# Kernel tuning notes

Hardware: AMD Instinct MI355X
Metric: run time of the kernel (lower is better)

## Reference

```python
import jax, jax.numpy as jnp
import numpy as np

QMIN, QMAX = -128.0, 127.0  # int8 range


def setup_inputs() -> dict:
    key = jax.random.key(0)
    k1, k2, k3 = jax.random.split(key, 3)
    B, S, IN, OUT = 4, 2048, 4096, 4096
    x = jax.random.normal(k1, (B, S, IN), dtype=jnp.float32)
    quantized_weight = jax.random.randint(k2, (OUT, IN), -128, 128, dtype=jnp.int32)
    weight_scale = jnp.float32(0.01)
    activation_scale = jnp.float32(0.05)
    bias = jax.random.normal(k3, (OUT,), dtype=jnp.float32)
    return {
        "x": x,
        "quantized_weight": quantized_weight,
        "weight_scale": weight_scale,
        "activation_scale": activation_scale,
        "bias": bias,
    }


def reference(x, quantized_weight, weight_scale, activation_scale, bias):
    # Fake-quantize activations to int8 grid (round, clamp), then dequantize.
    x_q = jnp.clip(jnp.round(x / activation_scale), QMIN, QMAX)
    x_f = x_q * activation_scale  # [B,S,IN] fp32
    # Dequantize int8 weights.
    w_f = quantized_weight.astype(jnp.float32) * weight_scale  # [OUT,IN]
    # F.linear: x @ W^T + b
    out = jnp.einsum("bsi,oi->bso", x_f, w_f) + bias
    return out
```

## Files before the change

kernel.cpp:

```cpp
#include <hip/hip_runtime.h>


#define MD 8192
#define ND 4096
#define KD 4096
#define KT (KD / 64)

typedef int   int4v   __attribute__((ext_vector_type(4)));
typedef float float4v __attribute__((ext_vector_type(4)));


__device__ __forceinline__ int quant1(float v, float s) {
  float q = rintf(v / s);
  q = fmaxf(-128.0f, fminf(127.0f, q));
  return ((int)q) & 0xff;
}

__global__ __launch_bounds__(256) void quant_x_kernel(
    const float* __restrict__ x, const float* __restrict__ as_p,
    signed char* __restrict__ aq) {
  const float s = as_p[0];
  int tid  = blockIdx.x * 256 + threadIdx.x;
  int sub  = tid >> 6;
  int lane = tid & 63;
  int mt = sub / KT;
  int kt = sub - mt * KT;
  int m = mt * 16 + (lane & 15);
  int k = kt * 64 + (lane >> 4) * 16;
  const float* src = x + (size_t)m * KD + k;
  int4v o;
#pragma unroll
  for (int i = 0; i < 4; ++i) {
    float4v v = *(const float4v*)(src + i * 4);
    o[i] = quant1(v.x, s) | (quant1(v.y, s) << 8) |
           (quant1(v.z, s) << 16) | (quant1(v.w, s) << 24);
  }
  *(int4v*)(aq + (size_t)sub * 1024 + lane * 16) = o;
}

__global__ __launch_bounds__(256) void pack_w_kernel(
    const int* __restrict__ w, signed char* __restrict__ wq) {
  int tid  = blockIdx.x * 256 + threadIdx.x;
  int sub  = tid >> 6;
  int lane = tid & 63;
  int nt = sub / KT;
  int kt = sub - nt * KT;
  int n = nt * 16 + (lane & 15);
  int k = kt * 64 + (lane >> 4) * 16;
  const int* src = w + (size_t)n * KD + k;
  int4v o;
#pragma unroll
  for (int i = 0; i < 4; ++i) {
    int4v v = *(const int4v*)(src + i * 4);
    o[i] = (v.x & 0xff) | ((v.y & 0xff) << 8) |
           ((v.z & 0xff) << 16) | ((v.w & 0xff) << 24);
  }
  *(int4v*)(wq + (size_t)sub * 1024 + lane * 16) = o;
}

__global__ __launch_bounds__(256) void gemm_i8_kernel(
    const signed char* __restrict__ aq, const signed char* __restrict__ wq,
    const float* __restrict__ ws_p, const float* __restrict__ as_p,
    const float* __restrict__ bias, float* __restrict__ out) {
  __shared__ signed char lds_a[8192];
  __shared__ signed char lds_b[8192];

  int nwg = gridDim.x;
  int cpx = nwg >> 3;
  int bid = blockIdx.x;
  int wg  = (bid & 7) * cpx + (bid >> 3);
  const int NT = ND / 128;
  int tm = wg / NT;
  int tn = wg - tm * NT;

  int tid  = threadIdx.x;
  int lane = tid & 63;
  int wv   = tid >> 6;
  int wr   = wv >> 1;
  int wc   = wv & 1;

  const size_t a_base = (size_t)(tm * 8) * KT * 1024;
  const size_t b_base = (size_t)(tn * 8) * KT * 1024;

  int4v acc[4][4];
#pragma unroll
  for (int i = 0; i < 4; ++i)
#pragma unroll
    for (int j = 0; j < 4; ++j) acc[i][j] = (int4v){0, 0, 0, 0};

  for (int kt = 0; kt < KT; ++kt) {
#pragma unroll
    for (int j = 0; j < 2; ++j) {
      int ia = wv + j * 4;
      const signed char* ga = aq + a_base + ((size_t)ia * KT + kt) * 1024 + lane * 16;
      __builtin_amdgcn_global_load_lds(
          (const __attribute__((address_space(1))) void*)ga,
          (__attribute__((address_space(3))) void*)(lds_a + ia * 1024), 16, 0, 0);
      const signed char* gb = wq + b_base + ((size_t)ia * KT + kt) * 1024 + lane * 16;
      __builtin_amdgcn_global_load_lds(
          (const __attribute__((address_space(1))) void*)gb,
          (__attribute__((address_space(3))) void*)(lds_b + ia * 1024), 16, 0, 0);
    }
    __syncthreads();

    int4v afrag[4], bfrag[4];
#pragma unroll
    for (int rb = 0; rb < 4; ++rb)
      afrag[rb] = *(const int4v*)(lds_a + (wr * 4 + rb) * 1024 + lane * 16);
#pragma unroll
    for (int cb = 0; cb < 4; ++cb)
      bfrag[cb] = *(const int4v*)(lds_b + (wc * 4 + cb) * 1024 + lane * 16);

#pragma unroll
    for (int rb = 0; rb < 4; ++rb)
#pragma unroll
      for (int cb = 0; cb < 4; ++cb)
        acc[rb][cb] = __builtin_amdgcn_mfma_i32_16x16x64_i8(
            afrag[rb], bfrag[cb], acc[rb][cb], 0, 0, 0);

    __syncthreads();
  }

  float scale = ws_p[0] * as_p[0];
  int col0 = tn * 128 + wc * 64 + (lane & 15);
  int row0 = tm * 128 + wr * 64 + ((lane >> 4) << 2);
  float bv[4];
#pragma unroll
  for (int cb = 0; cb < 4; ++cb) bv[cb] = bias[col0 + cb * 16];
#pragma unroll
  for (int rb = 0; rb < 4; ++rb) {
#pragma unroll
    for (int cb = 0; cb < 4; ++cb) {
      int col = col0 + cb * 16;
#pragma unroll
      for (int j = 0; j < 4; ++j) {
        int row = row0 + rb * 16 + j;
        out[(size_t)row * ND + col] = (float)acc[rb][cb][j] * scale + bv[cb];
      }
    }
  }
}

extern "C" void kernel_launch(void* const* d_in, const int* in_sizes, int n_in,
                              void* d_out, int out_size, void* d_ws, size_t ws_size,
                              hipStream_t stream) {
  const float* x    = (const float*)d_in[0];
  const int*   qw   = (const int*)d_in[1];
  const float* wsc  = (const float*)d_in[2];
  const float* asc  = (const float*)d_in[3];
  const float* bias = (const float*)d_in[4];
  float* out = (float*)d_out;

  signed char* aq = (signed char*)d_ws;
  signed char* wq = aq + (size_t)MD * KD;

  quant_x_kernel<<<(MD * KD / 16) / 256, 256, 0, stream>>>(x, asc, aq);
  pack_w_kernel<<<(ND * KD / 16) / 256, 256, 0, stream>>>(qw, wq);
  gemm_i8_kernel<<<(MD / 128) * (ND / 128), 256, 0, stream>>>(aq, wq, wsc, asc, bias, out);
}
```

Baseline: 431.5 us.

## Coalesce quant and pack kernels via LDS-staged swizzled transpose

The activation-quantize and weight-pack kernels now read contiguous row segments (each wave reads a 1KB-contiguous row chunk) instead of scattered 64-byte pieces per lane. They stage the packed bytes in a 16KB LDS tile with an XOR swizzle, then write out the MFMA-fragment layout in coalesced 16-byte stores. This targets the poor global-load coalescing of the preprocessing passes, which stream 128MB of x and 64MB of weights. It adds an LDS round trip and a barrier per block.

```diff
diff --git a/kernel.cpp b/kernel.cpp
--- a/kernel.cpp
+++ b/kernel.cpp
@@ -10,52 +10,78 @@
 typedef float float4v __attribute__((ext_vector_type(4)));
 
 
-__device__ __forceinline__ int quant1(float v, float s) {
+__device__ __forceinline__ unsigned int quant1(float v, float s) {
   float q = rintf(v / s);
   q = fmaxf(-128.0f, fminf(127.0f, q));
-  return ((int)q) & 0xff;
+  return ((unsigned int)(int)q) & 0xffu;
 }
 
 __global__ __launch_bounds__(256) void quant_x_kernel(
     const float* __restrict__ x, const float* __restrict__ as_p,
     signed char* __restrict__ aq) {
+  __shared__ unsigned int lds[4096];
   const float s = as_p[0];
-  int tid  = blockIdx.x * 256 + threadIdx.x;
-  int sub  = tid >> 6;
-  int lane = tid & 63;
-  int mt = sub / KT;
-  int kt = sub - mt * KT;
-  int m = mt * 16 + (lane & 15);
-  int k = kt * 64 + (lane >> 4) * 16;
-  const float* src = x + (size_t)m * KD + k;
-  int4v o;
+  int bid = blockIdx.x;
+  int r0 = (bid >> 4) * 64;
+  int k0 = (bid & 15) * 256;
+  int tid = threadIdx.x, lane = tid & 63, wv = tid >> 6;
+
+  int subL = wv * 4 + (lane >> 4);
+  int kgroup = (lane & 15) >> 2;
+  int c = lane & 3;
+  int X = subL * 4 + kgroup;
+  int xm = X & 15;
+  const float* src = x + (size_t)(r0 + wv * 16) * KD + k0 + lane * 4;
 #pragma unroll
-  for (int i = 0; i < 4; ++i) {
-    float4v v = *(const float4v*)(src + i * 4);
-    o[i] = quant1(v.x, s) | (quant1(v.y, s) << 8) |
-           (quant1(v.z, s) << 16) | (quant1(v.w, s) << 24);
+  for (int i = 0; i < 16; ++i) {
+    float4v v = *(const float4v*)(src + (size_t)i * KD);
+    unsigned int d = quant1(v.x, s) | (quant1(v.y, s) << 8) |
+                     (quant1(v.z, s) << 16) | (quant1(v.w, s) << 24);
+    lds[X * 64 + ((i ^ xm) << 2) + c] = d;
   }
-  *(int4v*)(aq + (size_t)sub * 1024 + lane * 16) = o;
+  __syncthreads();
+
+  size_t obase = ((size_t)(r0 >> 4) * KT + (k0 >> 6)) * 1024;
+  int y = tid & 15;
+#pragma unroll
+  for (int a = 0; a < 4; ++a) {
+    int Xr = (a * 4 + (tid >> 6)) * 4 + ((tid & 63) >> 4);
+    int4v vv = *(const int4v*)((const char*)lds + Xr * 256 + ((y ^ (Xr & 15)) << 4));
+    *(int4v*)(aq + obase + (size_t)a * KT * 1024 + tid * 16) = vv;
+  }
 }
 
 __global__ __launch_bounds__(256) void pack_w_kernel(
     const int* __restrict__ w, signed char* __restrict__ wq) {
-  int tid  = blockIdx.x * 256 + threadIdx.x;
-  int sub  = tid >> 6;
-  int lane = tid & 63;
-  int nt = sub / KT;
-  int kt = sub - nt * KT;
-  int n = nt * 16 + (lane & 15);
-  int k = kt * 64 + (lane >> 4) * 16;
-  const int* src = w + (size_t)n * KD + k;
-  int4v o;
+  __shared__ unsigned int lds[4096];
+  int bid = blockIdx.x;
+  int r0 = (bid >> 4) * 64;
+  int k0 = (bid & 15) * 256;
+  int tid = threadIdx.x, lane = tid & 63, wv = tid >> 6;
+
+  int subL = wv * 4 + (lane >> 4);
+  int kgroup = (lane & 15) >> 2;
+  int c = lane & 3;
+  int X = subL * 4 + kgroup;
+  int xm = X & 15;
+  const int* src = w + (size_t)(r0 + wv * 16) * KD + k0 + lane * 4;
 #pragma unroll
-  for (int i = 0; i < 4; ++i) {
-    int4v v = *(const int4v*)(src + i * 4);
-    o[i] = (v.x & 0xff) | ((v.y & 0xff) << 8) |
-           ((v.z & 0xff) << 16) | ((v.w & 0xff) << 24);
+  for (int i = 0; i < 16; ++i) {
+    int4v v = *(const int4v*)(src + (size_t)i * KD);
+    unsigned int d = (v.x & 0xff) | ((v.y & 0xff) << 8) |
+                     ((v.z & 0xff) << 16) | ((v.w & 0xff) << 24);
+    lds[X * 64 + ((i ^ xm) << 2) + c] = d;
   }
-  *(int4v*)(wq + (size_t)sub * 1024 + lane * 16) = o;
+  __syncthreads();
+
+  size_t obase = ((size_t)(r0 >> 4) * KT + (k0 >> 6)) * 1024;
+  int y = tid & 15;
+#pragma unroll
+  for (int a = 0; a < 4; ++a) {
+    int Xr = (a * 4 + (tid >> 6)) * 4 + ((tid & 63) >> 4);
+    int4v vv = *(const int4v*)((const char*)lds + Xr * 256 + ((y ^ (Xr & 15)) << 4));
+    *(int4v*)(wq + obase + (size_t)a * KT * 1024 + tid * 16) = vv;
+  }
 }
 
 __global__ __launch_bounds__(256) void gemm_i8_kernel(
@@ -154,7 +180,7 @@
   signed char* aq = (signed char*)d_ws;
   signed char* wq = aq + (size_t)MD * KD;
 
-  quant_x_kernel<<<(MD * KD / 16) / 256, 256, 0, stream>>>(x, asc, aq);
-  pack_w_kernel<<<(ND * KD / 16) / 256, 256, 0, stream>>>(qw, wq);
+  quant_x_kernel<<<(MD / 64) * (KD / 256), 256, 0, stream>>>(x, asc, aq);
+  pack_w_kernel<<<(ND / 64) * (KD / 256), 256, 0, stream>>>(qw, wq);
   gemm_i8_kernel<<<(MD / 128) * (ND / 128), 256, 0, stream>>>(aq, wq, wsc, asc, bias, out);
 }
```

Result: faster. 411.5 us (-4.7%).
